# Kernel optimization log

Measured on AMD Instinct MI355X. Metric: run time of the kernel, lower is better.

## Reference

```python
import jax, jax.numpy as jnp
import numpy as np

N_NODES = 100000
N_EDGES = 1600000
IN_CH = 128
OUT_CH = 64
HID = 2 * OUT_CH  # 128


def _glorot(key, fan_in, fan_out):
    s = np.sqrt(6.0 / (fan_in + fan_out)).astype(np.float32)
    return jax.random.uniform(key, (fan_in, fan_out), jnp.float32, -s, s)


def setup_inputs() -> dict:
    key = jax.random.key(0)
    ks = jax.random.split(key, 8)
    x = jax.random.normal(ks[0], (N_NODES, IN_CH), jnp.float32)
    edge_index = jax.random.randint(ks[1], (2, N_EDGES), 0, N_NODES, jnp.int32)
    return {
        "x": x,
        "edge_index": edge_index,
        "W1": _glorot(ks[2], IN_CH, HID),
        "b1": jnp.zeros((HID,), jnp.float32),
        "W_mu": _glorot(ks[3], HID, OUT_CH),
        "b_mu": jnp.zeros((OUT_CH,), jnp.float32),
        "W_ls": _glorot(ks[4], HID, OUT_CH),
        "b_ls": jnp.zeros((OUT_CH,), jnp.float32),
    }


def _gcn_layer(x, W, b, src, dst, norm, n):
    # transform -> gather -> edge-normalize -> scatter-add -> bias
    h = x @ W                                   # [N, F_out]
    msg = h[src] * norm[:, None]                # [E+N, F_out]
    agg = jax.ops.segment_sum(msg, dst, num_segments=n)
    return agg + b


def reference(x, edge_index, W1, b1, W_mu, b_mu, W_ls, b_ls):
    n = x.shape[0]
    loops = jnp.arange(n, dtype=edge_index.dtype)
    src = jnp.concatenate([edge_index[0], loops])  # self-loops appended
    dst = jnp.concatenate([edge_index[1], loops])
    # symmetric GCN normalization: deg computed at dst (incl. self-loops)
    deg = jax.ops.segment_sum(jnp.ones_like(dst, x.dtype), dst, num_segments=n)
    dinv = jnp.where(deg > 0, jax.lax.rsqrt(jnp.maximum(deg, 1.0)), 0.0)
    norm = dinv[src] * dinv[dst]                # cached=True: reused by all 3 layers

    h = jax.nn.relu(_gcn_layer(x, W1, b1, src, dst, norm, n))
    # dropout in eval mode -> identity
    mu = _gcn_layer(h, W_mu, b_mu, src, dst, norm, n)
    logstd = _gcn_layer(h, W_ls, b_ls, src, dst, norm, n)
    return mu, logstd
```

## Files before the change

kernel.cpp:

```cpp
#include <hip/hip_runtime.h>
#include <hip/hip_fp16.h>


#define NBUCKET 1024
#define NPB 512

typedef _Float16 half8_t __attribute__((ext_vector_type(8)));
typedef float f32x4_t __attribute__((ext_vector_type(4)));

__global__ __launch_bounds__(256) void hist_pass(const int* __restrict__ dst, int E,
                                                 int chunk, int shift,
                                                 int* __restrict__ blk_hist) {
    __shared__ int hist[NBUCKET];
    for (int i = threadIdx.x; i < NBUCKET; i += 256) hist[i] = 0;
    __syncthreads();
    int b = blockIdx.x;
    int beg = b * chunk;
    int end = beg + chunk; if (end > E) end = E;
    for (int i = beg + threadIdx.x; i < end; i += 256)
        atomicAdd(&hist[dst[i] >> shift], 1);
    __syncthreads();
    for (int i = threadIdx.x; i < NBUCKET; i += 256)
        blk_hist[(size_t)b * NBUCKET + i] = hist[i];
}

__global__ __launch_bounds__(256) void col_scan(const int* __restrict__ blk_hist,
                                                int* __restrict__ blk_base,
                                                int* __restrict__ bucket_total) {
    __shared__ int sh[256];
    int q = blockIdx.x, t = threadIdx.x;
    int v0 = blk_hist[(size_t)(2 * t) * NBUCKET + q];
    int v1 = blk_hist[(size_t)(2 * t + 1) * NBUCKET + q];
    int s = v0 + v1;
    sh[t] = s;
    __syncthreads();
    for (int off = 1; off < 256; off <<= 1) {
        int x = (t >= off) ? sh[t - off] : 0;
        __syncthreads();
        sh[t] += x;
        __syncthreads();
    }
    int pre = sh[t] - s;
    blk_base[(size_t)(2 * t) * NBUCKET + q] = pre;
    blk_base[(size_t)(2 * t + 1) * NBUCKET + q] = pre + v0;
    if (t == 255) bucket_total[q] = sh[255];
}

__global__ __launch_bounds__(256) void scan_bucket(const int* __restrict__ total,
                                                   int* __restrict__ base) {
    __shared__ int sh[256];
    int t = threadIdx.x;
    int idx0 = t * 4;
    int v[4];
#pragma unroll
    for (int k = 0; k < 4; ++k) v[k] = total[idx0 + k];
    int s = v[0] + v[1] + v[2] + v[3];
    sh[t] = s;
    __syncthreads();
    for (int off = 1; off < 256; off <<= 1) {
        int x = (t >= off) ? sh[t - off] : 0;
        __syncthreads();
        sh[t] += x;
        __syncthreads();
    }
    int run = sh[t] - s;
#pragma unroll
    for (int k = 0; k < 4; ++k) {
        base[idx0 + k] = run;
        run += v[k];
    }
}

__global__ __launch_bounds__(256) void scatter_pass(const int* __restrict__ src,
                                                    const int* __restrict__ dst, int E,
                                                    int chunk, int shift,
                                                    const int* __restrict__ bucket_base,
                                                    const int* __restrict__ blk_base,
                                                    long long* __restrict__ part) {
    __shared__ int cur[NBUCKET];
    int b = blockIdx.x;
    for (int i = threadIdx.x; i < NBUCKET; i += 256)
        cur[i] = bucket_base[i] + blk_base[(size_t)b * NBUCKET + i];
    __syncthreads();
    int beg = b * chunk;
    int end = beg + chunk; if (end > E) end = E;
    for (int i = beg + threadIdx.x; i < end; i += 256) {
        int d = dst[i], s = src[i];
        int q = d >> shift;
        int p = atomicAdd(&cur[q], 1);
        part[p] = ((long long)(unsigned)d << 32) | (unsigned)s;
    }
}

__global__ __launch_bounds__(256) void bucket_count(const long long* __restrict__ part,
                                                    const int* __restrict__ bucket_base,
                                                    const int* __restrict__ bucket_total,
                                                    int N, int shift,
                                                    int* __restrict__ degi,
                                                    float* __restrict__ dinv,
                                                    int* __restrict__ padded_total) {
    __shared__ int cnt[128];
    __shared__ int sh[128];
    int b = blockIdx.x, t = threadIdx.x;
    if (t < 128) cnt[t] = 0;
    __syncthreads();
    int node0 = b << shift;
    int beg = bucket_base[b];
    int end = beg + bucket_total[b];
    for (int i = beg + t; i < end; i += 256) {
        int d = (int)((unsigned long long)part[i] >> 32);
        atomicAdd(&cnt[d - node0], 1);
    }
    __syncthreads();
    if (t < 128) {
        int node = node0 + t;
        int c = (node < N) ? cnt[t] : 0;
        if (node < N) {
            degi[node] = c;
            dinv[node] = rsqrtf((float)(c + 1));
        }
        sh[t] = c;
    }
    __syncthreads();
    int padded = 0;
    if (t < 128) {
        int node = node0 + t;
        if (node < N) {
            int mine = (sh[t] + 15) >> 4;
            int pi = t ^ 1;
            int pnode = node0 + pi;
            int theirs = (pnode < N) ? ((sh[pi] + 15) >> 4) : 0;
            int L = mine > theirs ? mine : theirs;
            padded = L << 4;
        }
    }
    __syncthreads();
    if (t < 128) sh[t] = padded;
    __syncthreads();
    for (int off = 64; off >= 1; off >>= 1) {
        if (t < off) sh[t] += sh[t + off];
        __syncthreads();
    }
    if (t == 0) padded_total[b] = sh[0];
}

__global__ __launch_bounds__(256) void bucket_fill(const long long* __restrict__ part,
                                                   const int* __restrict__ bucket_base,
                                                   const int* __restrict__ bucket_total,
                                                   const int* __restrict__ padded_base,
                                                   const int* __restrict__ degi,
                                                   const float* __restrict__ dinv,
                                                   int N, int shift,
                                                   int* __restrict__ row_ptr,
                                                   long long* __restrict__ csr2) {
    __shared__ int sh[128];
    __shared__ int pexcl[128];
    __shared__ int padarr[128];
    __shared__ int cur[128];
    __shared__ float dvl[128];
    int b = blockIdx.x, t = threadIdx.x;
    int node0 = b << shift;
    int pbase = padded_base[b];

    if (t < 128) {
        int node = node0 + t;
        int deg = (node < N) ? degi[node] : 0;
        dvl[t] = (node < N) ? dinv[node] : 0.0f;
        sh[t] = deg;
    }
    __syncthreads();
    int padded = 0;
    if (t < 128) {
        int node = node0 + t;
        if (node < N) {
            int mine = (sh[t] + 15) >> 4;
            int pi = t ^ 1;
            int pnode = node0 + pi;
            int theirs = (pnode < N) ? ((sh[pi] + 15) >> 4) : 0;
            int L = mine > theirs ? mine : theirs;
            padded = L << 4;
        }
        padarr[t] = padded;
    }
    __syncthreads();
    if (t < 128) sh[t] = padded;
    __syncthreads();
    for (int off = 1; off < 128; off <<= 1) {
        int x = 0;
        if (t < 128 && t >= off) x = sh[t - off];
        __syncthreads();
        if (t < 128) sh[t] += x;
        __syncthreads();
    }
    if (t < 128) {
        int excl = sh[t] - padarr[t];
        pexcl[t] = excl;
        cur[t] = pbase + excl;
        int node = node0 + t;
        if (node < N) row_ptr[node] = pbase + excl;
    }
    __syncthreads();
    if (t == 0) {
        int boundary = node0 + 128;
        if (boundary > N) boundary = N;
        row_ptr[boundary] = pbase + sh[127];
    }
    int ebeg = bucket_base[b];
    int eend = ebeg + bucket_total[b];
    for (int i = ebeg + t; i < eend; i += 256) {
        long long pr = part[i];
        int d = (int)((unsigned long long)pr >> 32);
        int s = (int)(unsigned)(pr & 0xffffffffLL);
        int dl = d - node0;
        int p = atomicAdd(&cur[dl], 1);
        float w = dinv[s] * dvl[dl];
        csr2[p] = (long long)(unsigned)s |
                  ((long long)(unsigned)__float_as_uint(w) << 32);
    }
    __syncthreads();
    if (t < 128) {
        int node = node0 + t;
        if (node < N) {
            int endp = pbase + pexcl[t] + padarr[t];
            long long rec = (long long)(unsigned)node;
            for (int p = cur[t]; p < endp; ++p) csr2[p] = rec;
        }
    }
}

__global__ __launch_bounds__(256) void wprep(const float* __restrict__ W1,
                                             const float* __restrict__ Wmu,
                                             const float* __restrict__ bmu,
                                             const float* __restrict__ Wls,
                                             const float* __restrict__ bls,
                                             __half* __restrict__ Wt1,
                                             __half* __restrict__ Wt2,
                                             float* __restrict__ bias2) {
    int i = blockIdx.x * 256 + threadIdx.x;
    if (i < 16384) {
        int n = i >> 7, k = i & 127;
        Wt1[i] = __float2half_rn(W1[k * 128 + n]);
        float v = (n < 64) ? Wmu[k * 64 + n] : Wls[k * 64 + (n - 64)];
        Wt2[i] = __float2half_rn(v);
    }
    if (i < 64) {
        bias2[i] = bmu[i];
        bias2[64 + i] = bls[i];
    }
}

template <int AF32>
__global__ __launch_bounds__(256) void gemm_mfma(const void* __restrict__ Av, int M,
                                                 const __half* __restrict__ Bt,
                                                 __half* __restrict__ C) {
    __shared__ __half Bs[128][136];
    int tid = threadIdx.x;
#pragma unroll
    for (int i = 0; i < 8; ++i) {
        int idx = tid + i * 256;
        int r = idx >> 4;
        int c8 = (idx & 15) << 3;
        *(float4*)&Bs[r][c8] = *(const float4*)(Bt + r * 128 + c8);
    }
    __syncthreads();
    int wave = tid >> 6, lane = tid & 63;
    int lr = lane & 15, lk = lane >> 4;
    int row0 = blockIdx.x * 128 + wave * 32;

    f32x4_t acc[2][8];
#pragma unroll
    for (int rt = 0; rt < 2; ++rt)
#pragma unroll
        for (int ct = 0; ct < 8; ++ct) acc[rt][ct] = (f32x4_t)0.0f;

    half8_t afr[2][4];
#pragma unroll
    for (int rt = 0; rt < 2; ++rt) {
        int row = row0 + rt * 16 + lr;
        if (row >= M) row = M - 1;
        if (AF32) {
            const float* A = (const float*)Av + (size_t)row * 128;
#pragma unroll
            for (int ks = 0; ks < 4; ++ks) {
                float4 v0 = *(const float4*)(A + ks * 32 + lk * 8);
                float4 v1 = *(const float4*)(A + ks * 32 + lk * 8 + 4);
                half8_t f;
                f[0] = (_Float16)v0.x; f[1] = (_Float16)v0.y;
                f[2] = (_Float16)v0.z; f[3] = (_Float16)v0.w;
                f[4] = (_Float16)v1.x; f[5] = (_Float16)v1.y;
                f[6] = (_Float16)v1.z; f[7] = (_Float16)v1.w;
                afr[rt][ks] = f;
            }
        } else {
            const __half* A = (const __half*)Av + (size_t)row * 128;
#pragma unroll
            for (int ks = 0; ks < 4; ++ks)
                afr[rt][ks] = *(const half8_t*)(A + ks * 32 + lk * 8);
        }
    }
#pragma unroll
    for (int ks = 0; ks < 4; ++ks)
#pragma unroll
        for (int ct = 0; ct < 8; ++ct) {
            half8_t b = *(const half8_t*)&Bs[ct * 16 + lr][ks * 32 + lk * 8];
            acc[0][ct] = __builtin_amdgcn_mfma_f32_16x16x32_f16(afr[0][ks], b, acc[0][ct], 0, 0, 0);
            acc[1][ct] = __builtin_amdgcn_mfma_f32_16x16x32_f16(afr[1][ks], b, acc[1][ct], 0, 0, 0);
        }
#pragma unroll
    for (int rt = 0; rt < 2; ++rt)
#pragma unroll
        for (int r = 0; r < 4; ++r) {
            int row = row0 + rt * 16 + lk * 4 + r;
            if (row < M) {
#pragma unroll
                for (int ct = 0; ct < 8; ++ct)
                    C[(size_t)row * 128 + ct * 16 + lr] = __float2half_rn(acc[rt][ct][r]);
            }
        }
}

template <int MODE>
__global__ __launch_bounds__(256) void gather_pair(const __half* __restrict__ h,
                                                   const float* __restrict__ dinv,
                                                   const int* __restrict__ row_ptr,
                                                   const long long* __restrict__ csr2,
                                                   const float* __restrict__ bias,
                                                   void* __restrict__ outv, int n) {
    int wv = (blockIdx.x * 256 + threadIdx.x) >> 6;
    int lane = threadIdx.x & 63;
    int nodeA = wv * 2;
    if (nodeA >= n) return;
    int half = lane >> 5;
    int grp2 = (lane >> 4) & 1;
    int cs = lane & 15;
    int bvalid = (nodeA + 1) < n;
    int wid = nodeA + (half & bvalid);
    float dv = dinv[wid];
    int beg = row_ptr[wid];
    int end = row_ptr[wid + 1];

    float acc[8];
    {
        float4 raw = *(const float4*)(h + (size_t)wid * 128 + cs * 8);
        const __half2* hp = (const __half2*)&raw;
        float sw = (grp2 == 0) ? dv * dv : 0.0f;
#pragma unroll
        for (int q = 0; q < 4; ++q) {
            float2 f = __half22float2(hp[q]);
            acc[2 * q]     = sw * f.x;
            acc[2 * q + 1] = sw * f.y;
        }
    }

    long long e[8];
    if (beg < end) {
#pragma unroll
        for (int u = 0; u < 8; ++u) e[u] = csr2[beg + u * 2 + grp2];
    }
#pragma unroll 1
    for (int j = beg; j < end; j += 16) {
        int jn = j + 16;
        int jp = (jn < end) ? jn : beg;
        long long en[8];
#pragma unroll
        for (int u = 0; u < 8; ++u) en[u] = csr2[jp + u * 2 + grp2];
        float4 raw[8];
        float wgt[8];
#pragma unroll
        for (int u = 0; u < 8; ++u) {
            int s = (int)(unsigned)(e[u] & 0xffffffffLL);
            wgt[u] = __uint_as_float((unsigned)((unsigned long long)e[u] >> 32));
            raw[u] = *(const float4*)(h + (size_t)s * 128 + cs * 8);
        }
#pragma unroll
        for (int u = 0; u < 8; ++u) {
            const __half2* hp = (const __half2*)&raw[u];
#pragma unroll
            for (int q = 0; q < 4; ++q) {
                float2 f = __half22float2(hp[q]);
                acc[2 * q]     = fmaf(wgt[u], f.x, acc[2 * q]);
                acc[2 * q + 1] = fmaf(wgt[u], f.y, acc[2 * q + 1]);
            }
        }
#pragma unroll
        for (int u = 0; u < 8; ++u) e[u] = en[u];
    }

#pragma unroll
    for (int q = 0; q < 8; ++q) acc[q] += __shfl_xor(acc[q], 16, 64);

    {
        const float4* bp = (const float4*)(bias + cs * 8);
        float4 b0 = bp[0], b1 = bp[1];
        if (MODE == 0) {
            acc[0] = fmaxf(acc[0] + b0.x, 0.0f);
            acc[1] = fmaxf(acc[1] + b0.y, 0.0f);
            acc[2] = fmaxf(acc[2] + b0.z, 0.0f);
            acc[3] = fmaxf(acc[3] + b0.w, 0.0f);
            acc[4] = fmaxf(acc[4] + b1.x, 0.0f);
            acc[5] = fmaxf(acc[5] + b1.y, 0.0f);
            acc[6] = fmaxf(acc[6] + b1.z, 0.0f);
            acc[7] = fmaxf(acc[7] + b1.w, 0.0f);
        } else {
            acc[0] += b0.x; acc[1] += b0.y; acc[2] += b0.z; acc[3] += b0.w;
            acc[4] += b1.x; acc[5] += b1.y; acc[6] += b1.z; acc[7] += b1.w;
        }
    }

    if ((lane & 31) < 16 && (half == 0 || bvalid)) {
        if (MODE == 0) {
            union { __half2 h2[4]; float4 f4; } u;
            u.h2[0] = __floats2half2_rn(acc[0], acc[1]);
            u.h2[1] = __floats2half2_rn(acc[2], acc[3]);
            u.h2[2] = __floats2half2_rn(acc[4], acc[5]);
            u.h2[3] = __floats2half2_rn(acc[6], acc[7]);
            *(float4*)((__half*)outv + (size_t)wid * 128 + cs * 8) = u.f4;
        } else {
            float* mu = (float*)outv;
            float* ls = mu + (size_t)n * 64;
            float* op = (cs < 8) ? (mu + (size_t)wid * 64 + cs * 8)
                                 : (ls + (size_t)wid * 64 + (cs - 8) * 8);
            ((float4*)op)[0] = make_float4(acc[0], acc[1], acc[2], acc[3]);
            ((float4*)op)[1] = make_float4(acc[4], acc[5], acc[6], acc[7]);
        }
    }
}

extern "C" void kernel_launch(void* const* d_in, const int* in_sizes, int n_in,
                              void* d_out, int out_size, void* d_ws, size_t ws_size,
                              hipStream_t stream) {
    const float* x   = (const float*)d_in[0];
    const int*  eidx = (const int*)d_in[1];
    const float* W1  = (const float*)d_in[2];
    const float* b1  = (const float*)d_in[3];
    const float* Wmu = (const float*)d_in[4];
    const float* bmu = (const float*)d_in[5];
    const float* Wls = (const float*)d_in[6];
    const float* bls = (const float*)d_in[7];
    float* out = (float*)d_out;

    const int N = in_sizes[0] / 128;
    const int E = in_sizes[1] / 2;
    const int* src = eidx;
    const int* dst = eidx + E;

    int shift = 0;
    while (((N - 1) >> shift) >= NBUCKET) ++shift;
    int chunk = (E + NPB - 1) / NPB;

    char* w = (char*)d_ws;
    size_t off = 0;
    auto alloc = [&](size_t bytes) {
        void* p = w + off;
        off += (bytes + 255) & ~(size_t)255;
        return p;
    };
    int*       row_ptr      = (int*)alloc((size_t)(N + 1) * 4);
    float*     dinv         = (float*)alloc((size_t)N * 4);
    int*       bucket_total = (int*)alloc(NBUCKET * 4);
    int*       bucket_base  = (int*)alloc(NBUCKET * 4);
    int*       padded_total = (int*)alloc(NBUCKET * 4);
    int*       padded_base  = (int*)alloc(NBUCKET * 4);
    __half*    Wt1          = (__half*)alloc(16384 * 2);
    __half*    Wt2          = (__half*)alloc(16384 * 2);
    float*     bias2        = (float*)alloc(128 * 4);
    size_t csr_cap = (size_t)E + 31u * (size_t)N + 64;
    long long* csr2         = (long long*)alloc(csr_cap * 8);
    __half*    h1           = (__half*)alloc((size_t)N * 128 * 2);
    size_t Dstart = off;
    int*       degi     = (int*)alloc((size_t)N * 4);
    int*       blk_hist = (int*)alloc((size_t)NPB * NBUCKET * 4);
    int*       blk_base = (int*)alloc((size_t)NPB * NBUCKET * 4);
    long long* part     = (long long*)alloc((size_t)E * 8);
    size_t Dearly_end = off;
    __half* h = (__half*)(w + Dstart);
    __half* p = (__half*)(w + Dstart);
    size_t Dend = Dstart + (size_t)N * 128 * 2;
    off = (Dearly_end > Dend) ? Dearly_end : Dend;
    if (off > ws_size) return;

    wprep<<<64, 256, 0, stream>>>(W1, Wmu, bmu, Wls, bls, Wt1, Wt2, bias2);
    hist_pass<<<NPB, 256, 0, stream>>>(dst, E, chunk, shift, blk_hist);
    col_scan<<<NBUCKET, 256, 0, stream>>>(blk_hist, blk_base, bucket_total);
    scan_bucket<<<1, 256, 0, stream>>>(bucket_total, bucket_base);
    scatter_pass<<<NPB, 256, 0, stream>>>(src, dst, E, chunk, shift, bucket_base, blk_base, part);
    bucket_count<<<NBUCKET, 256, 0, stream>>>(part, bucket_base, bucket_total, N, shift,
                                              degi, dinv, padded_total);
    scan_bucket<<<1, 256, 0, stream>>>(padded_total, padded_base);
    bucket_fill<<<NBUCKET, 256, 0, stream>>>(part, bucket_base, bucket_total, padded_base,
                                             degi, dinv, N, shift, row_ptr, csr2);

    int gemm_blocks = (N + 127) / 128;
    int gblocks = (((N + 1) / 2) * 64 + 255) / 256;
    gemm_mfma<1><<<gemm_blocks, 256, 0, stream>>>(x, N, Wt1, h);
    gather_pair<0><<<gblocks, 256, 0, stream>>>(h, dinv, row_ptr, csr2, b1, h1, N);
    gemm_mfma<0><<<gemm_blocks, 256, 0, stream>>>(h1, N, Wt2, p);
    gather_pair<1><<<gblocks, 256, 0, stream>>>(p, dinv, row_ptr, csr2, bias2, out, N);
}
```

Baseline: 242.4 us.

## Store features in 16-column slices and gather per slice with folded self-loops

```diff
diff --git a/kernel.cpp b/kernel.cpp
--- a/kernel.cpp
+++ b/kernel.cpp
@@ -126,10 +126,10 @@
     if (t < 128) {
         int node = node0 + t;
         if (node < N) {
-            int mine = (sh[t] + 15) >> 4;
+            int mine = (sh[t] + 16) >> 4;
             int pi = t ^ 1;
             int pnode = node0 + pi;
-            int theirs = (pnode < N) ? ((sh[pi] + 15) >> 4) : 0;
+            int theirs = (pnode < N) ? ((sh[pi] + 16) >> 4) : 0;
             int L = mine > theirs ? mine : theirs;
             padded = L << 4;
         }
@@ -173,10 +173,10 @@
     if (t < 128) {
         int node = node0 + t;
         if (node < N) {
-            int mine = (sh[t] + 15) >> 4;
+            int mine = (sh[t] + 16) >> 4;
             int pi = t ^ 1;
             int pnode = node0 + pi;
-            int theirs = (pnode < N) ? ((sh[pi] + 15) >> 4) : 0;
+            int theirs = (pnode < N) ? ((sh[pi] + 16) >> 4) : 0;
             int L = mine > theirs ? mine : theirs;
             padded = L << 4;
         }
@@ -195,9 +195,16 @@
     if (t < 128) {
         int excl = sh[t] - padarr[t];
         pexcl[t] = excl;
-        cur[t] = pbase + excl;
-        int node = node0 + t;
-        if (node < N) row_ptr[node] = pbase + excl;
+        int node = node0 + t;
+        if (node < N) {
+            row_ptr[node] = pbase + excl;
+            float ws = dvl[t] * dvl[t];
+            csr2[pbase + excl] = (long long)(unsigned)node |
+                                 ((long long)(unsigned)__float_as_uint(ws) << 32);
+            cur[t] = pbase + excl + 1;
+        } else {
+            cur[t] = pbase + excl;
+        }
     }
     __syncthreads();
     if (t == 0) {
@@ -292,10 +299,12 @@
                 afr[rt][ks] = f;
             }
         } else {
-            const __half* A = (const __half*)Av + (size_t)row * 128;
-#pragma unroll
-            for (int ks = 0; ks < 4; ++ks)
-                afr[rt][ks] = *(const half8_t*)(A + ks * 32 + lk * 8);
+            const __half* A = (const __half*)Av;
+#pragma unroll
+            for (int ks = 0; ks < 4; ++ks) {
+                int slice = 2 * ks + (lk >> 1);
+                afr[rt][ks] = *(const half8_t*)(A + ((size_t)slice * M + row) * 16 + (lk & 1) * 8);
+            }
         }
     }
 #pragma unroll
@@ -314,114 +323,88 @@
             if (row < M) {
 #pragma unroll
                 for (int ct = 0; ct < 8; ++ct)
-                    C[(size_t)row * 128 + ct * 16 + lr] = __float2half_rn(acc[rt][ct][r]);
+                    C[((size_t)ct * M + row) * 16 + lr] = __float2half_rn(acc[rt][ct][r]);
             }
         }
 }
 
 template <int MODE>
-__global__ __launch_bounds__(256) void gather_pair(const __half* __restrict__ h,
-                                                   const float* __restrict__ dinv,
-                                                   const int* __restrict__ row_ptr,
-                                                   const long long* __restrict__ csr2,
-                                                   const float* __restrict__ bias,
-                                                   void* __restrict__ outv, int n) {
-    int wv = (blockIdx.x * 256 + threadIdx.x) >> 6;
-    int lane = threadIdx.x & 63;
-    int nodeA = wv * 2;
-    if (nodeA >= n) return;
-    int half = lane >> 5;
-    int grp2 = (lane >> 4) & 1;
-    int cs = lane & 15;
-    int bvalid = (nodeA + 1) < n;
-    int wid = nodeA + (half & bvalid);
-    float dv = dinv[wid];
-    int beg = row_ptr[wid];
-    int end = row_ptr[wid + 1];
-
-    float acc[8];
+__global__ __launch_bounds__(256) void gather_slice(const __half* __restrict__ hs,
+                                                    const int* __restrict__ row_ptr,
+                                                    const long long* __restrict__ csr2,
+                                                    const float* __restrict__ bias,
+                                                    void* __restrict__ outv, int N) {
+    int b = blockIdx.x;
+    int s = b & 7;
+    int node0 = (b >> 3) << 7;
+    int tid = threadIdx.x;
+    int wave = tid >> 6, lane = tid & 63;
+    int nd = lane >> 5;
+    int slot = (lane >> 1) & 15;
+    int ch = lane & 1;
+    const __half* hb = hs + (size_t)s * N * 16;
+    float bs[8];
     {
-        float4 raw = *(const float4*)(h + (size_t)wid * 128 + cs * 8);
-        const __half2* hp = (const __half2*)&raw;
-        float sw = (grp2 == 0) ? dv * dv : 0.0f;
-#pragma unroll
-        for (int q = 0; q < 4; ++q) {
-            float2 f = __half22float2(hp[q]);
-            acc[2 * q]     = sw * f.x;
-            acc[2 * q + 1] = sw * f.y;
-        }
-    }
-
-    long long e[8];
-    if (beg < end) {
-#pragma unroll
-        for (int u = 0; u < 8; ++u) e[u] = csr2[beg + u * 2 + grp2];
+        const float4* bp = (const float4*)(bias + s * 16 + ch * 8);
+        float4 b0 = bp[0], b1v = bp[1];
+        bs[0] = b0.x; bs[1] = b0.y; bs[2] = b0.z; bs[3] = b0.w;
+        bs[4] = b1v.x; bs[5] = b1v.y; bs[6] = b1v.z; bs[7] = b1v.w;
     }
 #pragma unroll 1
-    for (int j = beg; j < end; j += 16) {
-        int jn = j + 16;
-        int jp = (jn < end) ? jn : beg;
-        long long en[8];
-#pragma unroll
-        for (int u = 0; u < 8; ++u) en[u] = csr2[jp + u * 2 + grp2];
-        float4 raw[8];
-        float wgt[8];
-#pragma unroll
-        for (int u = 0; u < 8; ++u) {
-            int s = (int)(unsigned)(e[u] & 0xffffffffLL);
-            wgt[u] = __uint_as_float((unsigned)((unsigned long long)e[u] >> 32));
-            raw[u] = *(const float4*)(h + (size_t)s * 128 + cs * 8);
-        }
-#pragma unroll
-        for (int u = 0; u < 8; ++u) {
-            const __half2* hp = (const __half2*)&raw[u];
+    for (int pr = wave; pr < 64; pr += 4) {
+        int nodeA = node0 + pr * 2;
+        if (nodeA >= N) break;
+        int bval = (nodeA + 1) < N;
+        int wid = nodeA + (nd & bval);
+        int beg = row_ptr[wid];
+        int end = row_ptr[wid + 1];
+        float acc[8] = {};
+        long long e = csr2[beg + slot];
+#pragma unroll 1
+        for (int j = beg; j < end; j += 16) {
+            int jn = j + 16;
+            long long en = 0;
+            if (jn < end) en = csr2[jn + slot];
+            int src = (int)(unsigned)(e & 0xffffffffLL);
+            float wgt = __uint_as_float((unsigned)((unsigned long long)e >> 32));
+            float4 raw = *(const float4*)(hb + (size_t)src * 16 + ch * 8);
+            const __half2* hp = (const __half2*)&raw;
 #pragma unroll
             for (int q = 0; q < 4; ++q) {
                 float2 f = __half22float2(hp[q]);
-                acc[2 * q]     = fmaf(wgt[u], f.x, acc[2 * q]);
-                acc[2 * q + 1] = fmaf(wgt[u], f.y, acc[2 * q + 1]);
+                acc[2 * q]     = fmaf(wgt, f.x, acc[2 * q]);
+                acc[2 * q + 1] = fmaf(wgt, f.y, acc[2 * q + 1]);
             }
-        }
-#pragma unroll
-        for (int u = 0; u < 8; ++u) e[u] = en[u];
-    }
-
-#pragma unroll
-    for (int q = 0; q < 8; ++q) acc[q] += __shfl_xor(acc[q], 16, 64);
-
-    {
-        const float4* bp = (const float4*)(bias + cs * 8);
-        float4 b0 = bp[0], b1 = bp[1];
-        if (MODE == 0) {
-            acc[0] = fmaxf(acc[0] + b0.x, 0.0f);
-            acc[1] = fmaxf(acc[1] + b0.y, 0.0f);
-            acc[2] = fmaxf(acc[2] + b0.z, 0.0f);
-            acc[3] = fmaxf(acc[3] + b0.w, 0.0f);
-            acc[4] = fmaxf(acc[4] + b1.x, 0.0f);
-            acc[5] = fmaxf(acc[5] + b1.y, 0.0f);
-            acc[6] = fmaxf(acc[6] + b1.z, 0.0f);
-            acc[7] = fmaxf(acc[7] + b1.w, 0.0f);
-        } else {
-            acc[0] += b0.x; acc[1] += b0.y; acc[2] += b0.z; acc[3] += b0.w;
-            acc[4] += b1.x; acc[5] += b1.y; acc[6] += b1.z; acc[7] += b1.w;
-        }
-    }
-
-    if ((lane & 31) < 16 && (half == 0 || bvalid)) {
-        if (MODE == 0) {
-            union { __half2 h2[4]; float4 f4; } u;
-            u.h2[0] = __floats2half2_rn(acc[0], acc[1]);
-            u.h2[1] = __floats2half2_rn(acc[2], acc[3]);
-            u.h2[2] = __floats2half2_rn(acc[4], acc[5]);
-            u.h2[3] = __floats2half2_rn(acc[6], acc[7]);
-            *(float4*)((__half*)outv + (size_t)wid * 128 + cs * 8) = u.f4;
-        } else {
-            float* mu = (float*)outv;
-            float* ls = mu + (size_t)n * 64;
-            float* op = (cs < 8) ? (mu + (size_t)wid * 64 + cs * 8)
-                                 : (ls + (size_t)wid * 64 + (cs - 8) * 8);
-            ((float4*)op)[0] = make_float4(acc[0], acc[1], acc[2], acc[3]);
-            ((float4*)op)[1] = make_float4(acc[4], acc[5], acc[6], acc[7]);
+            e = en;
+        }
+#pragma unroll
+        for (int q = 0; q < 8; ++q) {
+            acc[q] += __shfl_xor(acc[q], 2, 64);
+            acc[q] += __shfl_xor(acc[q], 4, 64);
+            acc[q] += __shfl_xor(acc[q], 8, 64);
+            acc[q] += __shfl_xor(acc[q], 16, 64);
+        }
+        if (slot == 0 && (nd == 0 || bval)) {
+            if (MODE == 0) {
+#pragma unroll
+                for (int q = 0; q < 8; ++q) acc[q] = fmaxf(acc[q] + bs[q], 0.0f);
+                union { __half2 h2[4]; float4 f4; } u;
+                u.h2[0] = __floats2half2_rn(acc[0], acc[1]);
+                u.h2[1] = __floats2half2_rn(acc[2], acc[3]);
+                u.h2[2] = __floats2half2_rn(acc[4], acc[5]);
+                u.h2[3] = __floats2half2_rn(acc[6], acc[7]);
+                *(float4*)((__half*)outv + ((size_t)s * N + wid) * 16 + ch * 8) = u.f4;
+            } else {
+#pragma unroll
+                for (int q = 0; q < 8; ++q) acc[q] += bs[q];
+                int c0 = s * 16 + ch * 8;
+                float* mu = (float*)outv;
+                float* ls = mu + (size_t)N * 64;
+                float* dst = (c0 < 64) ? (mu + (size_t)wid * 64 + c0)
+                                       : (ls + (size_t)wid * 64 + (c0 - 64));
+                ((float4*)dst)[0] = make_float4(acc[0], acc[1], acc[2], acc[3]);
+                ((float4*)dst)[1] = make_float4(acc[4], acc[5], acc[6], acc[7]);
+            }
         }
     }
 }
@@ -464,7 +447,7 @@
     __half*    Wt1          = (__half*)alloc(16384 * 2);
     __half*    Wt2          = (__half*)alloc(16384 * 2);
     float*     bias2        = (float*)alloc(128 * 4);
-    size_t csr_cap = (size_t)E + 31u * (size_t)N + 64;
+    size_t csr_cap = (size_t)E + 40u * (size_t)N + 64;
     long long* csr2         = (long long*)alloc(csr_cap * 8);
     __half*    h1           = (__half*)alloc((size_t)N * 128 * 2);
     size_t Dstart = off;
@@ -491,9 +474,9 @@
                                              degi, dinv, N, shift, row_ptr, csr2);
 
     int gemm_blocks = (N + 127) / 128;
-    int gblocks = (((N + 1) / 2) * 64 + 255) / 256;
+    int gblocks = ((N + 127) / 128) * 8;
     gemm_mfma<1><<<gemm_blocks, 256, 0, stream>>>(x, N, Wt1, h);
-    gather_pair<0><<<gblocks, 256, 0, stream>>>(h, dinv, row_ptr, csr2, b1, h1, N);
+    gather_slice<0><<<gblocks, 256, 0, stream>>>(h, row_ptr, csr2, b1, h1, N);
     gemm_mfma<0><<<gemm_blocks, 256, 0, stream>>>(h1, N, Wt2, p);
-    gather_pair<1><<<gblocks, 256, 0, stream>>>(p, dinv, row_ptr, csr2, bias2, out, N);
-}
+    gather_slice<1><<<gblocks, 256, 0, stream>>>(p, row_ptr, csr2, bias2, out, N);
+}
```

After: 402.6 us. 1.66x slower.

## Fold weight prep into histogram and inline bucket scans to cut launches

Applied to the files above, without the earlier changes.

```diff
diff --git a/kernel.cpp b/kernel.cpp
--- a/kernel.cpp
+++ b/kernel.cpp
@@ -8,13 +8,35 @@
 typedef _Float16 half8_t __attribute__((ext_vector_type(8)));
 typedef float f32x4_t __attribute__((ext_vector_type(4)));
 
-__global__ __launch_bounds__(256) void hist_pass(const int* __restrict__ dst, int E,
+__global__ __launch_bounds__(256) void prep_hist(const int* __restrict__ dst, int E,
                                                  int chunk, int shift,
-                                                 int* __restrict__ blk_hist) {
+                                                 int* __restrict__ blk_hist,
+                                                 const float* __restrict__ W1,
+                                                 const float* __restrict__ Wmu,
+                                                 const float* __restrict__ bmu,
+                                                 const float* __restrict__ Wls,
+                                                 const float* __restrict__ bls,
+                                                 __half* __restrict__ Wt1,
+                                                 __half* __restrict__ Wt2,
+                                                 float* __restrict__ bias2) {
+    int b = blockIdx.x;
+    if (b >= NPB) {
+        int i = (b - NPB) * 256 + threadIdx.x;
+        if (i < 16384) {
+            int n = i >> 7, k = i & 127;
+            Wt1[i] = __float2half_rn(W1[k * 128 + n]);
+            float v = (n < 64) ? Wmu[k * 64 + n] : Wls[k * 64 + (n - 64)];
+            Wt2[i] = __float2half_rn(v);
+        }
+        if (i < 64) {
+            bias2[i] = bmu[i];
+            bias2[64 + i] = bls[i];
+        }
+        return;
+    }
     __shared__ int hist[NBUCKET];
     for (int i = threadIdx.x; i < NBUCKET; i += 256) hist[i] = 0;
     __syncthreads();
-    int b = blockIdx.x;
     int beg = b * chunk;
     int end = beg + chunk; if (end > E) end = E;
     for (int i = beg + threadIdx.x; i < end; i += 256)
@@ -46,45 +68,59 @@
     if (t == 255) bucket_total[q] = sh[255];
 }
 
-__global__ __launch_bounds__(256) void scan_bucket(const int* __restrict__ total,
-                                                   int* __restrict__ base) {
-    __shared__ int sh[256];
+__device__ __forceinline__ int partial_base(const int* __restrict__ total, int b,
+                                            int* sh ) {
     int t = threadIdx.x;
-    int idx0 = t * 4;
-    int v[4];
-#pragma unroll
-    for (int k = 0; k < 4; ++k) v[k] = total[idx0 + k];
-    int s = v[0] + v[1] + v[2] + v[3];
+    int s = 0;
+    for (int i = t; i < b; i += 256) s += total[i];
     sh[t] = s;
     __syncthreads();
-    for (int off = 1; off < 256; off <<= 1) {
-        int x = (t >= off) ? sh[t - off] : 0;
-        __syncthreads();
-        sh[t] += x;
-        __syncthreads();
-    }
-    int run = sh[t] - s;
-#pragma unroll
-    for (int k = 0; k < 4; ++k) {
-        base[idx0 + k] = run;
-        run += v[k];
-    }
+    for (int off = 128; off >= 1; off >>= 1) {
+        if (t < off) sh[t] += sh[t + off];
+        __syncthreads();
+    }
+    int r = sh[0];
+    __syncthreads();
+    return r;
 }
 
 __global__ __launch_bounds__(256) void scatter_pass(const int* __restrict__ src,
                                                     const int* __restrict__ dst, int E,
                                                     int chunk, int shift,
-                                                    const int* __restrict__ bucket_base,
+                                                    const int* __restrict__ bucket_total,
                                                     const int* __restrict__ blk_base,
                                                     long long* __restrict__ part) {
     __shared__ int cur[NBUCKET];
-    int b = blockIdx.x;
-    for (int i = threadIdx.x; i < NBUCKET; i += 256)
-        cur[i] = bucket_base[i] + blk_base[(size_t)b * NBUCKET + i];
+    __shared__ int sh[256];
+    int b = blockIdx.x, t = threadIdx.x;
+    {
+        int idx0 = t * 4;
+        int v[4];
+#pragma unroll
+        for (int k = 0; k < 4; ++k) v[k] = bucket_total[idx0 + k];
+        int s = v[0] + v[1] + v[2] + v[3];
+        sh[t] = s;
+        __syncthreads();
+        for (int off = 1; off < 256; off <<= 1) {
+            int x = (t >= off) ? sh[t - off] : 0;
+            __syncthreads();
+            sh[t] += x;
+            __syncthreads();
+        }
+        int run = sh[t] - s;
+#pragma unroll
+        for (int k = 0; k < 4; ++k) {
+            cur[idx0 + k] = run;
+            run += v[k];
+        }
+    }
+    __syncthreads();
+    for (int i = t; i < NBUCKET; i += 256)
+        cur[i] += blk_base[(size_t)b * NBUCKET + i];
     __syncthreads();
     int beg = b * chunk;
     int end = beg + chunk; if (end > E) end = E;
-    for (int i = beg + threadIdx.x; i < end; i += 256) {
+    for (int i = beg + t; i < end; i += 256) {
         int d = dst[i], s = src[i];
         int q = d >> shift;
         int p = atomicAdd(&cur[q], 1);
@@ -93,20 +129,19 @@
 }
 
 __global__ __launch_bounds__(256) void bucket_count(const long long* __restrict__ part,
-                                                    const int* __restrict__ bucket_base,
                                                     const int* __restrict__ bucket_total,
                                                     int N, int shift,
                                                     int* __restrict__ degi,
                                                     float* __restrict__ dinv,
                                                     int* __restrict__ padded_total) {
     __shared__ int cnt[128];
-    __shared__ int sh[128];
+    __shared__ int sh[256];
     int b = blockIdx.x, t = threadIdx.x;
+    int beg = partial_base(bucket_total, b, sh);
+    int end = beg + bucket_total[b];
     if (t < 128) cnt[t] = 0;
     __syncthreads();
     int node0 = b << shift;
-    int beg = bucket_base[b];
-    int end = beg + bucket_total[b];
     for (int i = beg + t; i < end; i += 256) {
         int d = (int)((unsigned long long)part[i] >> 32);
         atomicAdd(&cnt[d - node0], 1);
@@ -135,7 +170,7 @@
         }
     }
     __syncthreads();
-    if (t < 128) sh[t] = padded;
+    if (t < 128) sh[t] = padded; else if (t < 256) sh[t] = 0;
     __syncthreads();
     for (int off = 64; off >= 1; off >>= 1) {
         if (t < off) sh[t] += sh[t + off];
@@ -145,22 +180,23 @@
 }
 
 __global__ __launch_bounds__(256) void bucket_fill(const long long* __restrict__ part,
-                                                   const int* __restrict__ bucket_base,
                                                    const int* __restrict__ bucket_total,
-                                                   const int* __restrict__ padded_base,
+                                                   const int* __restrict__ padded_total,
                                                    const int* __restrict__ degi,
                                                    const float* __restrict__ dinv,
                                                    int N, int shift,
                                                    int* __restrict__ row_ptr,
                                                    long long* __restrict__ csr2) {
-    __shared__ int sh[128];
+    __shared__ int sh[256];
     __shared__ int pexcl[128];
     __shared__ int padarr[128];
     __shared__ int cur[128];
     __shared__ float dvl[128];
     int b = blockIdx.x, t = threadIdx.x;
     int node0 = b << shift;
-    int pbase = padded_base[b];
+    int ebeg = partial_base(bucket_total, b, sh);
+    int eend = ebeg + bucket_total[b];
+    int pbase = partial_base(padded_total, b, sh);
 
     if (t < 128) {
         int node = node0 + t;
@@ -205,8 +241,6 @@
         if (boundary > N) boundary = N;
         row_ptr[boundary] = pbase + sh[127];
     }
-    int ebeg = bucket_base[b];
-    int eend = ebeg + bucket_total[b];
     for (int i = ebeg + t; i < eend; i += 256) {
         long long pr = part[i];
         int d = (int)((unsigned long long)pr >> 32);
@@ -225,27 +259,6 @@
             long long rec = (long long)(unsigned)node;
             for (int p = cur[t]; p < endp; ++p) csr2[p] = rec;
         }
-    }
-}
-
-__global__ __launch_bounds__(256) void wprep(const float* __restrict__ W1,
-                                             const float* __restrict__ Wmu,
-                                             const float* __restrict__ bmu,
-                                             const float* __restrict__ Wls,
-                                             const float* __restrict__ bls,
-                                             __half* __restrict__ Wt1,
-                                             __half* __restrict__ Wt2,
-                                             float* __restrict__ bias2) {
-    int i = blockIdx.x * 256 + threadIdx.x;
-    if (i < 16384) {
-        int n = i >> 7, k = i & 127;
-        Wt1[i] = __float2half_rn(W1[k * 128 + n]);
-        float v = (n < 64) ? Wmu[k * 64 + n] : Wls[k * 64 + (n - 64)];
-        Wt2[i] = __float2half_rn(v);
-    }
-    if (i < 64) {
-        bias2[i] = bmu[i];
-        bias2[64 + i] = bls[i];
     }
 }
 
@@ -458,9 +471,7 @@
     int*       row_ptr      = (int*)alloc((size_t)(N + 1) * 4);
     float*     dinv         = (float*)alloc((size_t)N * 4);
     int*       bucket_total = (int*)alloc(NBUCKET * 4);
-    int*       bucket_base  = (int*)alloc(NBUCKET * 4);
     int*       padded_total = (int*)alloc(NBUCKET * 4);
-    int*       padded_base  = (int*)alloc(NBUCKET * 4);
     __half*    Wt1          = (__half*)alloc(16384 * 2);
     __half*    Wt2          = (__half*)alloc(16384 * 2);
     float*     bias2        = (float*)alloc(128 * 4);
@@ -479,15 +490,14 @@
     off = (Dearly_end > Dend) ? Dearly_end : Dend;
     if (off > ws_size) return;
 
-    wprep<<<64, 256, 0, stream>>>(W1, Wmu, bmu, Wls, bls, Wt1, Wt2, bias2);
-    hist_pass<<<NPB, 256, 0, stream>>>(dst, E, chunk, shift, blk_hist);
+    prep_hist<<<NPB + 64, 256, 0, stream>>>(dst, E, chunk, shift, blk_hist,
+                                            W1, Wmu, bmu, Wls, bls, Wt1, Wt2, bias2);
     col_scan<<<NBUCKET, 256, 0, stream>>>(blk_hist, blk_base, bucket_total);
-    scan_bucket<<<1, 256, 0, stream>>>(bucket_total, bucket_base);
-    scatter_pass<<<NPB, 256, 0, stream>>>(src, dst, E, chunk, shift, bucket_base, blk_base, part);
-    bucket_count<<<NBUCKET, 256, 0, stream>>>(part, bucket_base, bucket_total, N, shift,
+    scatter_pass<<<NPB, 256, 0, stream>>>(src, dst, E, chunk, shift,
+                                          bucket_total, blk_base, part);
+    bucket_count<<<NBUCKET, 256, 0, stream>>>(part, bucket_total, N, shift,
                                               degi, dinv, padded_total);
-    scan_bucket<<<1, 256, 0, stream>>>(padded_total, padded_base);
-    bucket_fill<<<NBUCKET, 256, 0, stream>>>(part, bucket_base, bucket_total, padded_base,
+    bucket_fill<<<NBUCKET, 256, 0, stream>>>(part, bucket_total, padded_total,
                                              degi, dinv, N, shift, row_ptr, csr2);
 
     int gemm_blocks = (N + 127) / 128;
```

After: 236.3 us. 1.03x faster.
